# Optimization experiments

Hardware: AMD Instinct MI355X
Metric: run time of the kernel (lower is better)

Reference implementation:

```python
import jax, jax.numpy as jnp
import numpy as np
import math

B, S, D, H = 2, 2048, 1024, 16
DH = D // H  # head_size = 64


def setup_inputs() -> dict:
    key = jax.random.key(0)
    ks = jax.random.split(key, 11)
    s = 0.02
    return {
        "queries": jax.random.normal(ks[0], (B, S, D), jnp.float32),
        "keys": jax.random.normal(ks[1], (B, S, D), jnp.float32),
        "values": jax.random.normal(ks[2], (B, S, D), jnp.float32),
        # nn.Linear weights: y = x @ W.T + b, W has shape (out, in)
        "W_Q": jax.random.normal(ks[3], (D, D), jnp.float32) * s,
        "b_Q": jax.random.normal(ks[4], (D,), jnp.float32) * s,
        "W_K": jax.random.normal(ks[5], (D, D), jnp.float32) * s,
        "b_K": jax.random.normal(ks[6], (D,), jnp.float32) * s,
        "W_V": jax.random.normal(ks[7], (D, D), jnp.float32) * s,
        "b_V": jax.random.normal(ks[8], (D,), jnp.float32) * s,
        "W_O": jax.random.normal(ks[9], (D, D), jnp.float32) * s,
        "b_O": jax.random.normal(ks[10], (D,), jnp.float32) * s,
    }


def _split_heads(x):
    # (B, S, H*DH) -> (B, H, S, DH); torch.chunk+stack == reshape+transpose
    b, s, _ = x.shape
    return x.reshape(b, s, H, DH).transpose(0, 2, 1, 3)


def reference(queries, keys, values, W_Q, b_Q, W_K, b_K, W_V, b_V, W_O, b_O):
    q = _split_heads(queries @ W_Q.T + b_Q)  # (B,H,S,DH)
    k = _split_heads(keys @ W_K.T + b_K)
    v = _split_heads(values @ W_V.T + b_V)

    scale = 1.0 / math.sqrt(DH)
    scores = jnp.einsum("bhqd,bhkd->bhqk", q, k) * scale  # (B,H,S,S)
    causal = jnp.tril(jnp.ones((S, S), dtype=bool))  # allow j <= i (causal)
    scores = jnp.where(causal, scores, -jnp.inf)
    weights = jax.nn.softmax(scores, axis=-1)

    attended = jnp.einsum("bhqk,bhkd->bhqd", weights, v)  # (B,H,S,DH)
    merged = attended.transpose(0, 2, 1, 3).reshape(B, S, D)  # merge_heads
    return merged @ W_O.T + b_O
```

## Files before the change

kernel.cpp:

```cpp
#include <hip/hip_runtime.h>


typedef __bf16 bf16x8 __attribute__((ext_vector_type(8)));
typedef float  f32x4  __attribute__((ext_vector_type(4)));

#define B_  2
#define S_  2048
#define D_  1024
#define H_  16
#define DH_ 64

#define NEG_ 1.0e30f
#define M2_  5.77078016f
#define QSCALE_ 0.18033688f

#if __has_builtin(__builtin_amdgcn_exp2f)
#define EXP2(x) __builtin_amdgcn_exp2f(x)
#else
#define EXP2(x) __builtin_exp2f(x)
#endif

__device__ __forceinline__ void load_lds16(const __bf16* g, __bf16* lds_base) {
    __builtin_amdgcn_global_load_lds(
        (const __attribute__((address_space(1))) void*)g,
        (__attribute__((address_space(3))) void*)lds_base,
        16, 0, 0);
}

__device__ __forceinline__ bf16x8 cvt8(const float* __restrict__ p) {
    const float4 a = *(const float4*)p;
    const float4 b = *(const float4*)(p + 4);
    bf16x8 r;
    r[0] = (__bf16)a.x; r[1] = (__bf16)a.y; r[2] = (__bf16)a.z; r[3] = (__bf16)a.w;
    r[4] = (__bf16)b.x; r[5] = (__bf16)b.y; r[6] = (__bf16)b.z; r[7] = (__bf16)b.w;
    return r;
}

__global__ void cvt_kernel(const float* __restrict__ q, const float* __restrict__ k,
                           const float* __restrict__ v,
                           const float* __restrict__ wq, const float* __restrict__ wk,
                           const float* __restrict__ wv, const float* __restrict__ wo,
                           __bf16* __restrict__ qb, __bf16* __restrict__ kb,
                           __bf16* __restrict__ vb,
                           __bf16* __restrict__ wqb, __bf16* __restrict__ wkb,
                           __bf16* __restrict__ wvb, __bf16* __restrict__ wob) {
    const int z = blockIdx.z;
    const float* src; __bf16* dst; size_t n;
    switch (z) {
        case 0: src = q;  dst = qb;  n = (size_t)B_ * S_ * D_; break;
        case 1: src = k;  dst = kb;  n = (size_t)B_ * S_ * D_; break;
        case 2: src = v;  dst = vb;  n = (size_t)B_ * S_ * D_; break;
        case 3: src = wq; dst = wqb; n = (size_t)D_ * D_; break;
        case 4: src = wk; dst = wkb; n = (size_t)D_ * D_; break;
        case 5: src = wv; dst = wvb; n = (size_t)D_ * D_; break;
        default: src = wo; dst = wob; n = (size_t)D_ * D_; break;
    }
    const size_t i = ((size_t)blockIdx.x * 256 + threadIdx.x) * 8;
    if (i >= n) return;
    *(bf16x8*)(dst + i) = cvt8(src + i);
}

__device__ __forceinline__ void gemm128_bf(const __bf16* __restrict__ X,
                                           const __bf16* __restrict__ W,
                                           int m0, int n0, int K,
                                           __bf16* As, __bf16* Bs,
                                           f32x4 acc[4][4]) {
    const int tid  = threadIdx.x;
    const int wave = tid >> 6, lane = tid & 63;
    const int row  = lane & 15, quad = lane >> 4;
    const int wm   = wave >> 1, wn = wave & 1;
    const int arow = lane >> 2;
    const int acol = (lane & 3) * 8;

    const f32x4 fzero = {0.f, 0.f, 0.f, 0.f};
#pragma unroll
    for (int mt = 0; mt < 4; ++mt)
#pragma unroll
        for (int nt = 0; nt < 4; ++nt) acc[mt][nt] = fzero;

    for (int k0 = 0; k0 < K; k0 += 32) {
#pragma unroll
        for (int c = 0; c < 2; ++c) {
            const int j = wave * 2 + c;
            load_lds16(X + (size_t)(m0 + j * 16 + arow) * K + k0 + acol, As + j * 512);
            load_lds16(W + (size_t)(n0 + j * 16 + arow) * K + k0 + acol, Bs + j * 512);
        }
        __syncthreads();
        bf16x8 af[4], bfv[4];
#pragma unroll
        for (int t = 0; t < 4; ++t) {
            af[t]  = *(const bf16x8*)(As + (wm * 64 + t * 16 + row) * 32 + quad * 8);
            bfv[t] = *(const bf16x8*)(Bs + (wn * 64 + t * 16 + row) * 32 + quad * 8);
        }
#pragma unroll
        for (int mt = 0; mt < 4; ++mt)
#pragma unroll
            for (int nt = 0; nt < 4; ++nt)
                acc[mt][nt] = __builtin_amdgcn_mfma_f32_16x16x32_bf16(
                    af[mt], bfv[nt], acc[mt][nt], 0, 0, 0);
        __syncthreads();
    }
}

__global__ void qkv_kernel(const __bf16* __restrict__ qb, const __bf16* __restrict__ kb,
                           const __bf16* __restrict__ vb,
                           const __bf16* __restrict__ wqb, const __bf16* __restrict__ wkb,
                           const __bf16* __restrict__ wvb,
                           const float* __restrict__ bq, const float* __restrict__ bk,
                           const float* __restrict__ bv,
                           __bf16* __restrict__ q_ws, __bf16* __restrict__ k_ws,
                           __bf16* __restrict__ v_ws) {
    __shared__ __align__(16) __bf16 As[128 * 32];
    __shared__ __align__(16) __bf16 Bs[128 * 32];
    const int mode = blockIdx.z;
    const __bf16* X    = mode == 0 ? qb : mode == 1 ? kb : vb;
    const __bf16* W    = mode == 0 ? wqb : mode == 1 ? wkb : wvb;
    const float*  bias = mode == 0 ? bq : mode == 1 ? bk : bv;
    const int m0 = blockIdx.y * 128, n0 = blockIdx.x * 128;

    f32x4 acc[4][4];
    gemm128_bf(X, W, m0, n0, D_, As, Bs, acc);

    const int tid = threadIdx.x;
    const int wave = tid >> 6, lane = tid & 63;
    const int row = lane & 15, quad = lane >> 4;
    const int wm = wave >> 1, wn = wave & 1;

#pragma unroll
    for (int nt = 0; nt < 4; ++nt) {
        const int n  = n0 + wn * 64 + nt * 16 + row;
        const float bf = bias[n];
        const int h = n >> 6, dh = n & 63;
#pragma unroll
        for (int mt = 0; mt < 4; ++mt) {
#pragma unroll
            for (int r = 0; r < 4; ++r) {
                const int m = m0 + wm * 64 + mt * 16 + quad * 4 + r;
                const int bb = m >> 11, s = m & (S_ - 1);
                const float val = acc[mt][nt][r] + bf;
                if (mode == 0)
                    q_ws[(((size_t)bb * H_ + h) * S_ + s) * DH_ + dh] = (__bf16)(val * QSCALE_);
                else if (mode == 1)
                    k_ws[(((size_t)bb * H_ + h) * S_ + s) * DH_ + dh] = (__bf16)val;
                else
                    v_ws[(((size_t)bb * H_ + h) * DH_ + dh) * S_ + s] = (__bf16)val;
            }
        }
    }
}

__global__ void attn_kernel(const __bf16* __restrict__ q_ws, const __bf16* __restrict__ k_ws,
                            const __bf16* __restrict__ v_ws, __bf16* __restrict__ att) {
    __shared__ __align__(16) __bf16 Ks[128 * 64];
    __shared__ __align__(16) __bf16 Vs[64 * 128];
    __shared__ __align__(16) __bf16 Ps[4 * 32 * 32];

    const int bh = blockIdx.x;
    const int qt = (S_ / 128 - 1) - blockIdx.y;
    const int tid = threadIdx.x, wave = tid >> 6, lane = tid & 63;
    const int row = lane & 15, quad = lane >> 4;

    const __bf16* Qg = q_ws + ((size_t)bh * S_ + qt * 128 + wave * 32) * DH_;
    const __bf16* Kg = k_ws + (size_t)bh * S_ * DH_;
    const __bf16* Vg = v_ws + (size_t)bh * DH_ * S_;
    __bf16* Pw = Ps + wave * 1024;

    bf16x8 qf[2][2];
#pragma unroll
    for (int mt = 0; mt < 2; ++mt)
#pragma unroll
        for (int ks = 0; ks < 2; ++ks)
            qf[mt][ks] = *(const bf16x8*)(Qg + (mt * 16 + row) * DH_ + ks * 32 + quad * 8);

    bf16x8 onesf;
#pragma unroll
    for (int i = 0; i < 8; ++i) onesf[i] = (__bf16)1.0f;

    const f32x4 fzero = {0.f, 0.f, 0.f, 0.f};
    f32x4 oacc[2][4];
    f32x4 lacc[2];
#pragma unroll
    for (int mt = 0; mt < 2; ++mt) {
#pragma unroll
        for (int dt = 0; dt < 4; ++dt) oacc[mt][dt] = fzero;
        lacc[mt] = fzero;
    }

    for (int kv = 0; kv <= qt; ++kv) {
#pragma unroll
        for (int c = 0; c < 4; ++c) {
            const int ck = wave * 4 + c;
            load_lds16(Kg + (size_t)kv * 128 * DH_ + ck * 512 + lane * 8, Ks + ck * 512);
            load_lds16(Vg + (size_t)(ck * 4 + (lane >> 4)) * S_ + kv * 128 + (lane & 15) * 8,
                       Vs + ck * 512);
        }
        __syncthreads();

        const bool diag = (kv == qt);
#pragma unroll
        for (int kc = 0; kc < 4; ++kc) {
            f32x4 s[2][2];
#pragma unroll
            for (int mt = 0; mt < 2; ++mt)
#pragma unroll
                for (int jn = 0; jn < 2; ++jn) s[mt][jn] = fzero;
#pragma unroll
            for (int jn = 0; jn < 2; ++jn) {
                const int nt = kc * 2 + jn;
                bf16x8 kf0 = *(const bf16x8*)(Ks + (nt * 16 + row) * DH_ + quad * 8);
                bf16x8 kf1 = *(const bf16x8*)(Ks + (nt * 16 + row) * DH_ + 32 + quad * 8);
#pragma unroll
                for (int mt = 0; mt < 2; ++mt) {
                    s[mt][jn] = __builtin_amdgcn_mfma_f32_16x16x32_bf16(qf[mt][0], kf0, s[mt][jn], 0, 0, 0);
                    s[mt][jn] = __builtin_amdgcn_mfma_f32_16x16x32_bf16(qf[mt][1], kf1, s[mt][jn], 0, 0, 0);
                }
            }

            if (diag) {
#pragma unroll
                for (int mt = 0; mt < 2; ++mt)
#pragma unroll
                    for (int jn = 0; jn < 2; ++jn) {
                        const int cloc = kc * 32 + jn * 16 + row;
#pragma unroll
                        for (int r = 0; r < 4; ++r) {
                            const int rloc = wave * 32 + mt * 16 + quad * 4 + r;
                            if (cloc > rloc) s[mt][jn][r] = -NEG_;
                        }
                    }
            }

#pragma unroll
            for (int mt = 0; mt < 2; ++mt)
#pragma unroll
                for (int r = 0; r < 4; ++r)
#pragma unroll
                    for (int jn = 0; jn < 2; ++jn) {
                        const float p = EXP2(s[mt][jn][r] - M2_);
                        Pw[(mt * 16 + quad * 4 + r) * 32 + jn * 16 + row] = (__bf16)p;
                    }

            bf16x8 pf0 = *(const bf16x8*)(Pw + (row) * 32 + quad * 8);
            bf16x8 pf1 = *(const bf16x8*)(Pw + (16 + row) * 32 + quad * 8);
#pragma unroll
            for (int dt = 0; dt < 4; ++dt) {
                bf16x8 vf = *(const bf16x8*)(Vs + (dt * 16 + row) * 128 + kc * 32 + quad * 8);
                oacc[0][dt] = __builtin_amdgcn_mfma_f32_16x16x32_bf16(pf0, vf, oacc[0][dt], 0, 0, 0);
                oacc[1][dt] = __builtin_amdgcn_mfma_f32_16x16x32_bf16(pf1, vf, oacc[1][dt], 0, 0, 0);
            }
            lacc[0] = __builtin_amdgcn_mfma_f32_16x16x32_bf16(pf0, onesf, lacc[0], 0, 0, 0);
            lacc[1] = __builtin_amdgcn_mfma_f32_16x16x32_bf16(pf1, onesf, lacc[1], 0, 0, 0);
        }
        __syncthreads();
    }

    const int b = bh >> 4, h = bh & 15;
#pragma unroll
    for (int mt = 0; mt < 2; ++mt) {
#pragma unroll
        for (int r = 0; r < 4; ++r) {
            const float inv = 1.f / lacc[mt][r];
            const int s = qt * 128 + wave * 32 + mt * 16 + quad * 4 + r;
#pragma unroll
            for (int dt = 0; dt < 4; ++dt) {
                att[((size_t)b * S_ + s) * D_ + h * DH_ + dt * 16 + row] =
                    (__bf16)(oacc[mt][dt][r] * inv);
            }
        }
    }
}

__global__ void oproj_kernel(const __bf16* __restrict__ attn, const __bf16* __restrict__ wob,
                             const float* __restrict__ bo, float* __restrict__ out) {
    __shared__ __align__(16) __bf16 As[128 * 32];
    __shared__ __align__(16) __bf16 Bs[128 * 32];
    const int m0 = blockIdx.y * 128, n0 = blockIdx.x * 128;

    f32x4 acc[4][4];
    gemm128_bf(attn, wob, m0, n0, D_, As, Bs, acc);

    const int tid = threadIdx.x;
    const int wave = tid >> 6, lane = tid & 63;
    const int row = lane & 15, quad = lane >> 4;
    const int wm = wave >> 1, wn = wave & 1;

#pragma unroll
    for (int nt = 0; nt < 4; ++nt) {
        const int n = n0 + wn * 64 + nt * 16 + row;
        const float bf = bo[n];
#pragma unroll
        for (int mt = 0; mt < 4; ++mt) {
#pragma unroll
            for (int r = 0; r < 4; ++r) {
                const int m = m0 + wm * 64 + mt * 16 + quad * 4 + r;
                out[(size_t)m * D_ + n] = acc[mt][nt][r] + bf;
            }
        }
    }
}

extern "C" void kernel_launch(void* const* d_in, const int* in_sizes, int n_in,
                              void* d_out, int out_size, void* d_ws, size_t ws_size,
                              hipStream_t stream) {
    const float* q_in = (const float*)d_in[0];
    const float* k_in = (const float*)d_in[1];
    const float* v_in = (const float*)d_in[2];
    const float* wq   = (const float*)d_in[3];
    const float* bq   = (const float*)d_in[4];
    const float* wk   = (const float*)d_in[5];
    const float* bk   = (const float*)d_in[6];
    const float* wv   = (const float*)d_in[7];
    const float* bv   = (const float*)d_in[8];
    const float* wo   = (const float*)d_in[9];
    const float* bo   = (const float*)d_in[10];

    char* ws = (char*)d_ws;
    const size_t MB = 1024 * 1024;
    __bf16* qb   = (__bf16*)(ws);
    __bf16* kb   = (__bf16*)(ws + 8 * MB);
    __bf16* vb   = (__bf16*)(ws + 16 * MB);
    __bf16* wqb  = (__bf16*)(ws + 24 * MB);
    __bf16* wkb  = (__bf16*)(ws + 26 * MB);
    __bf16* wvb  = (__bf16*)(ws + 28 * MB);
    __bf16* wob  = (__bf16*)(ws + 30 * MB);
    __bf16* q_ws = (__bf16*)(ws + 32 * MB);
    __bf16* k_ws = (__bf16*)(ws + 40 * MB);
    __bf16* v_ws = (__bf16*)(ws + 48 * MB);
    __bf16* attb = qb;
    float*  out  = (float*)d_out;

    cvt_kernel<<<dim3(2048, 1, 7), 256, 0, stream>>>(
        q_in, k_in, v_in, wq, wk, wv, wo, qb, kb, vb, wqb, wkb, wvb, wob);
    qkv_kernel<<<dim3(D_ / 128, (B_ * S_) / 128, 3), 256, 0, stream>>>(
        qb, kb, vb, wqb, wkb, wvb, bq, bk, bv, q_ws, k_ws, v_ws);
    attn_kernel<<<dim3(B_ * H_, S_ / 128), 256, 0, stream>>>(q_ws, k_ws, v_ws, attb);
    oproj_kernel<<<dim3(D_ / 128, (B_ * S_) / 128), 256, 0, stream>>>(attb, wob, bo, out);
}
```

Baseline: 244.7 us.

## Shrink attention query tile to 64, swizzle LDS, trim diagonal work, add setprio

The attention kernel now processes 64 query rows per block (16 per wave) instead of 128, doubling the grid to improve load balance and occupancy across CUs. On the diagonal KV tile it skips key chunks that are fully masked. K, V and P tiles in shared memory use XOR swizzles to avoid bank conflicts. It also adds launch bounds and s_setprio around the MFMA sections. The cost is that each K/V tile is loaded by twice as many blocks, which doubles K/V memory traffic and halves reuse of each tile.

Result: faster. 225.6 us (-7.8%).

```diff
diff --git a/kernel.cpp b/kernel.cpp
--- a/kernel.cpp
+++ b/kernel.cpp
@@ -149,123 +149,118 @@
     }
 }
 
-__global__ void attn_kernel(const __bf16* __restrict__ q_ws, const __bf16* __restrict__ k_ws,
-                            const __bf16* __restrict__ v_ws, __bf16* __restrict__ att) {
+__global__ __launch_bounds__(256, 4)
+void attn_kernel(const __bf16* __restrict__ q_ws, const __bf16* __restrict__ k_ws,
+                 const __bf16* __restrict__ v_ws, __bf16* __restrict__ att) {
     __shared__ __align__(16) __bf16 Ks[128 * 64];
     __shared__ __align__(16) __bf16 Vs[64 * 128];
-    __shared__ __align__(16) __bf16 Ps[4 * 32 * 32];
+    __shared__ __align__(16) __bf16 Ps[4 * 16 * 32];
 
     const int bh = blockIdx.x;
-    const int qt = (S_ / 128 - 1) - blockIdx.y;
+    const int qt = (S_ / 64 - 1) - blockIdx.y;
     const int tid = threadIdx.x, wave = tid >> 6, lane = tid & 63;
     const int row = lane & 15, quad = lane >> 4;
 
-    const __bf16* Qg = q_ws + ((size_t)bh * S_ + qt * 128 + wave * 32) * DH_;
+    const __bf16* Qg = q_ws + ((size_t)bh * S_ + qt * 64 + wave * 16) * DH_;
     const __bf16* Kg = k_ws + (size_t)bh * S_ * DH_;
     const __bf16* Vg = v_ws + (size_t)bh * DH_ * S_;
-    __bf16* Pw = Ps + wave * 1024;
-
-    bf16x8 qf[2][2];
-#pragma unroll
-    for (int mt = 0; mt < 2; ++mt)
-#pragma unroll
-        for (int ks = 0; ks < 2; ++ks)
-            qf[mt][ks] = *(const bf16x8*)(Qg + (mt * 16 + row) * DH_ + ks * 32 + quad * 8);
+    __bf16* Pw = Ps + wave * 512;
+
+    bf16x8 qf[2];
+#pragma unroll
+    for (int ks = 0; ks < 2; ++ks)
+        qf[ks] = *(const bf16x8*)(Qg + row * DH_ + ks * 32 + quad * 8);
 
     bf16x8 onesf;
 #pragma unroll
     for (int i = 0; i < 8; ++i) onesf[i] = (__bf16)1.0f;
 
     const f32x4 fzero = {0.f, 0.f, 0.f, 0.f};
-    f32x4 oacc[2][4];
-    f32x4 lacc[2];
-#pragma unroll
-    for (int mt = 0; mt < 2; ++mt) {
-#pragma unroll
-        for (int dt = 0; dt < 4; ++dt) oacc[mt][dt] = fzero;
-        lacc[mt] = fzero;
-    }
-
-    for (int kv = 0; kv <= qt; ++kv) {
+    f32x4 oacc[4];
+    f32x4 lacc;
+#pragma unroll
+    for (int dt = 0; dt < 4; ++dt) oacc[dt] = fzero;
+    lacc = fzero;
+
+    const int klsub = lane >> 3;
+    const int kcol  = ((lane & 7) ^ klsub) * 8;
+    const int nkv = (qt >> 1) + 1;
+
+    for (int kv = 0; kv < nkv; ++kv) {
 #pragma unroll
         for (int c = 0; c < 4; ++c) {
             const int ck = wave * 4 + c;
-            load_lds16(Kg + (size_t)kv * 128 * DH_ + ck * 512 + lane * 8, Ks + ck * 512);
-            load_lds16(Vg + (size_t)(ck * 4 + (lane >> 4)) * S_ + kv * 128 + (lane & 15) * 8,
-                       Vs + ck * 512);
+            const int krow = ck * 8 + klsub;
+            load_lds16(Kg + (size_t)(kv * 128 + krow) * DH_ + kcol, Ks + ck * 512);
+            const int vrow = ck * 4 + (lane >> 4);
+            const int vcol = ((lane & 15) ^ (vrow & 7)) * 8;
+            load_lds16(Vg + (size_t)vrow * S_ + kv * 128 + vcol, Vs + ck * 512);
         }
         __syncthreads();
 
-        const bool diag = (kv == qt);
-#pragma unroll
-        for (int kc = 0; kc < 4; ++kc) {
-            f32x4 s[2][2];
-#pragma unroll
-            for (int mt = 0; mt < 2; ++mt)
-#pragma unroll
-                for (int jn = 0; jn < 2; ++jn) s[mt][jn] = fzero;
+        const bool diag = (kv == nkv - 1);
+        const int kcend = diag ? ((qt & 1) ? 4 : 2) : 4;
+        const int swz = (row & 7) << 3;
+
+        for (int kc = 0; kc < kcend; ++kc) {
+            f32x4 s[2];
+            s[0] = fzero; s[1] = fzero;
+            __builtin_amdgcn_s_setprio(1);
 #pragma unroll
             for (int jn = 0; jn < 2; ++jn) {
                 const int nt = kc * 2 + jn;
-                bf16x8 kf0 = *(const bf16x8*)(Ks + (nt * 16 + row) * DH_ + quad * 8);
-                bf16x8 kf1 = *(const bf16x8*)(Ks + (nt * 16 + row) * DH_ + 32 + quad * 8);
-#pragma unroll
-                for (int mt = 0; mt < 2; ++mt) {
-                    s[mt][jn] = __builtin_amdgcn_mfma_f32_16x16x32_bf16(qf[mt][0], kf0, s[mt][jn], 0, 0, 0);
-                    s[mt][jn] = __builtin_amdgcn_mfma_f32_16x16x32_bf16(qf[mt][1], kf1, s[mt][jn], 0, 0, 0);
+                const int kb = (nt * 16 + row) * 64 + quad * 8;
+                bf16x8 kf0 = *(const bf16x8*)(Ks + (kb ^ swz));
+                bf16x8 kf1 = *(const bf16x8*)(Ks + ((kb + 32) ^ swz));
+                s[jn] = __builtin_amdgcn_mfma_f32_16x16x32_bf16(qf[0], kf0, s[jn], 0, 0, 0);
+                s[jn] = __builtin_amdgcn_mfma_f32_16x16x32_bf16(qf[1], kf1, s[jn], 0, 0, 0);
+            }
+            __builtin_amdgcn_s_setprio(0);
+
+            if (diag) {
+                const int rbase = (qt & 1) * 64;
+#pragma unroll
+                for (int jn = 0; jn < 2; ++jn) {
+                    const int cloc = kc * 32 + jn * 16 + row;
+#pragma unroll
+                    for (int r = 0; r < 4; ++r) {
+                        const int rloc = rbase + wave * 16 + quad * 4 + r;
+                        if (cloc > rloc) s[jn][r] = -NEG_;
+                    }
                 }
             }
 
-            if (diag) {
-#pragma unroll
-                for (int mt = 0; mt < 2; ++mt)
-#pragma unroll
-                    for (int jn = 0; jn < 2; ++jn) {
-                        const int cloc = kc * 32 + jn * 16 + row;
-#pragma unroll
-                        for (int r = 0; r < 4; ++r) {
-                            const int rloc = wave * 32 + mt * 16 + quad * 4 + r;
-                            if (cloc > rloc) s[mt][jn][r] = -NEG_;
-                        }
-                    }
-            }
-
-#pragma unroll
-            for (int mt = 0; mt < 2; ++mt)
-#pragma unroll
-                for (int r = 0; r < 4; ++r)
-#pragma unroll
-                    for (int jn = 0; jn < 2; ++jn) {
-                        const float p = EXP2(s[mt][jn][r] - M2_);
-                        Pw[(mt * 16 + quad * 4 + r) * 32 + jn * 16 + row] = (__bf16)p;
-                    }
-
-            bf16x8 pf0 = *(const bf16x8*)(Pw + (row) * 32 + quad * 8);
-            bf16x8 pf1 = *(const bf16x8*)(Pw + (16 + row) * 32 + quad * 8);
+#pragma unroll
+            for (int r = 0; r < 4; ++r)
+#pragma unroll
+                for (int jn = 0; jn < 2; ++jn) {
+                    const float p = EXP2(s[jn][r] - M2_);
+                    Pw[(((quad * 4 + r) * 32) + jn * 16 + row) ^ (quad << 3)] = (__bf16)p;
+                }
+
+            bf16x8 pf = *(const bf16x8*)(Pw + ((row * 32 + quad * 8) ^ (((row >> 2) & 3) << 3)));
+            __builtin_amdgcn_s_setprio(1);
 #pragma unroll
             for (int dt = 0; dt < 4; ++dt) {
-                bf16x8 vf = *(const bf16x8*)(Vs + (dt * 16 + row) * 128 + kc * 32 + quad * 8);
-                oacc[0][dt] = __builtin_amdgcn_mfma_f32_16x16x32_bf16(pf0, vf, oacc[0][dt], 0, 0, 0);
-                oacc[1][dt] = __builtin_amdgcn_mfma_f32_16x16x32_bf16(pf1, vf, oacc[1][dt], 0, 0, 0);
-            }
-            lacc[0] = __builtin_amdgcn_mfma_f32_16x16x32_bf16(pf0, onesf, lacc[0], 0, 0, 0);
-            lacc[1] = __builtin_amdgcn_mfma_f32_16x16x32_bf16(pf1, onesf, lacc[1], 0, 0, 0);
+                const int vb = (dt * 16 + row) * 128 + kc * 32 + quad * 8;
+                bf16x8 vf = *(const bf16x8*)(Vs + (vb ^ swz));
+                oacc[dt] = __builtin_amdgcn_mfma_f32_16x16x32_bf16(pf, vf, oacc[dt], 0, 0, 0);
+            }
+            lacc = __builtin_amdgcn_mfma_f32_16x16x32_bf16(pf, onesf, lacc, 0, 0, 0);
+            __builtin_amdgcn_s_setprio(0);
         }
         __syncthreads();
     }
 
     const int b = bh >> 4, h = bh & 15;
 #pragma unroll
-    for (int mt = 0; mt < 2; ++mt) {
-#pragma unroll
-        for (int r = 0; r < 4; ++r) {
-            const float inv = 1.f / lacc[mt][r];
-            const int s = qt * 128 + wave * 32 + mt * 16 + quad * 4 + r;
-#pragma unroll
-            for (int dt = 0; dt < 4; ++dt) {
-                att[((size_t)b * S_ + s) * D_ + h * DH_ + dt * 16 + row] =
-                    (__bf16)(oacc[mt][dt][r] * inv);
-            }
+    for (int r = 0; r < 4; ++r) {
+        const float inv = 1.f / lacc[r];
+        const int s = qt * 64 + wave * 16 + quad * 4 + r;
+#pragma unroll
+        for (int dt = 0; dt < 4; ++dt) {
+            att[((size_t)b * S_ + s) * D_ + h * DH_ + dt * 16 + row] =
+                (__bf16)(oacc[dt][r] * inv);
         }
     }
 }
@@ -333,6 +328,6 @@
         q_in, k_in, v_in, wq, wk, wv, wo, qb, kb, vb, wqb, wkb, wvb, wob);
     qkv_kernel<<<dim3(D_ / 128, (B_ * S_) / 128, 3), 256, 0, stream>>>(
         qb, kb, vb, wqb, wkb, wvb, bq, bk, bv, q_ws, k_ws, v_ws);
-    attn_kernel<<<dim3(B_ * H_, S_ / 128), 256, 0, stream>>>(q_ws, k_ws, v_ws, attb);
+    attn_kernel<<<dim3(B_ * H_, S_ / 64), 256, 0, stream>>>(q_ws, k_ws, v_ws, attb);
     oproj_kernel<<<dim3(D_ / 128, (B_ * S_) / 128), 256, 0, stream>>>(attb, wob, bo, out);
 }
```
